# Kernel tuning notes

Measured on AMD Instinct MI355X. Metric: run time of the kernel, lower is better.

## Reference

```python
import jax, jax.numpy as jnp
import numpy as np

NU0 = 1.0  # nu0 temperature floor


def setup_inputs() -> dict:
    key = jax.random.key(0)
    ks = jax.random.split(key, 12)
    N, E, P, L, IN, H = 20000, 320000, 50000, 20, 128, 64
    xavier = lambda k, s: jax.random.normal(k, s, jnp.float32) * np.sqrt(2.0 / (s[0] + s[1]))
    return {
        "x": jax.random.normal(ks[0], (N, IN), jnp.float32),
        "edge_index": jax.random.randint(ks[1], (2, E), 0, N),
        "pairs": jax.random.randint(ks[2], (P, 2), 0, N),
        "gumbel": jax.random.gumbel(ks[3], (L, P, 2), jnp.float32),
        "W_enc": xavier(ks[4], (IN, H)),
        "Omega": xavier(ks[5], (H, H)),
        "Ws_raw": xavier(ks[6], (H, H)),
        "W_fc1": xavier(ks[7], (2 * H, 2 * H)),
        "W_fc2": xavier(ks[8], (2 * H, 2)),
        "W_fv": xavier(ks[9], (2 * H, 1)),
        "W_p1": xavier(ks[10], (2 * H, H)),
        "W_p2": xavier(ks[11], (H, 1)),
    }


def reference(x, edge_index, pairs, gumbel, W_enc, Omega, Ws_raw, W_fc1, W_fc2, W_fv, W_p1, W_p2):
    N = x.shape[0]
    src, dst = pairs[:, 0], pairs[:, 1]
    # add self loops
    loops = jnp.arange(N)
    row = jnp.concatenate([edge_index[0], loops])
    col = jnp.concatenate([edge_index[1], loops])
    deg = jax.ops.segment_sum(jnp.ones(col.shape, x.dtype), col, num_segments=N)
    dinv = jnp.where(deg > 0, deg, 1.0) ** -0.5 * (deg > 0)
    norm = dinv[row] * dinv[col]  # [E+N]
    Omega_as = Omega - Omega.T            # antisymmetric part
    W_s = (Ws_raw + Ws_raw.T) * 0.5       # symmetric part

    H = jax.nn.relu(x @ W_enc)                         # [N, h]
    r = jnp.concatenate([H[src], H[dst]], axis=-1)     # [P, 2h]
    ts0 = jnp.zeros(pairs.shape[0], x.dtype)

    def step(carry, g):
        H, r, ts = carry
        anti = -jax.nn.relu(H @ Omega_as)
        msg = (H @ W_s)[row] * norm[:, None]           # gather + weight
        sym = jax.ops.segment_sum(msg, col, num_segments=N)  # scatter-add
        dH = jax.nn.relu(jnp.tanh(anti + sym))
        huv = jnp.concatenate([H[src], H[dst]], axis=-1)     # [P, 2h]
        logits = jax.nn.relu(huv @ W_fc1) @ W_fc2            # [P, 2]
        nu = jax.nn.softplus(huv @ W_fv) + NU0               # [P, 1]
        c = jax.nn.softmax((logits + g) / nu, axis=-1)       # soft gumbel-softmax
        tau = c[:, :1]
        dr = jnp.concatenate([dH[src], dH[dst]], axis=-1)
        r = r + tau * dr
        H = H + dH
        ts = ts + jax.lax.stop_gradient(tau[:, 0])
        return (H, r, ts), None

    (H, r, ts), _ = jax.lax.scan(step, (H, r, ts0), gumbel)
    scores = (jax.nn.relu(r @ W_p1) @ W_p2)[:, 0]
    return scores, ts
```

## Files before the change

kernel.cpp:

```cpp
#include <hip/hip_runtime.h>
#include <math.h>


typedef short bf16x8 __attribute__((ext_vector_type(8)));
typedef float f32x4 __attribute__((ext_vector_type(4)));
typedef unsigned short u16x8 __attribute__((ext_vector_type(8)));

__device__ __forceinline__ float bf2f(unsigned short u) {
  return __uint_as_float(((unsigned)u) << 16);
}
__device__ __forceinline__ unsigned short f2bf(float f) {
  unsigned u = __float_as_uint(f);
  unsigned r = (u + 0x7FFFu + ((u >> 16) & 1u)) >> 16;
  return (unsigned short)r;
}
__device__ __forceinline__ float softplusf(float x) {
  return x > 20.f ? x : log1pf(expf(x));
}


__global__ void count_kernel(const int* __restrict__ col, int E, int* __restrict__ cnt) {
  int e = blockIdx.x * blockDim.x + threadIdx.x;
  if (e < E) atomicAdd(&cnt[col[e]], 1);
}

__global__ __launch_bounds__(1024) void scan1_kernel(int* __restrict__ cnt,
                                                     int* __restrict__ colptr,
                                                     float* __restrict__ dinv,
                                                     int* __restrict__ bsum, int N) {
  __shared__ int sh[1024];
  int t = threadIdx.x, b = blockIdx.x;
  int i = b * 1024 + t;
  int v = (i < N) ? cnt[i] : 0;
  sh[t] = v;
  __syncthreads();
  for (int off = 1; off < 1024; off <<= 1) {
    int o = (t >= off) ? sh[t - off] : 0;
    __syncthreads();
    sh[t] += o;
    __syncthreads();
  }
  if (i < N) {
    colptr[i] = sh[t] - v;
    dinv[i] = rsqrtf((float)(v + 1));
    cnt[i] = 0;
  }
  if (t == 1023) bsum[b] = sh[1023];
}

__global__ void scan2_kernel(int* __restrict__ bsum, int B) {
  if (threadIdx.x == 0 && blockIdx.x == 0) {
    int run = 0;
    for (int b = 0; b < B; b++) {
      int x = bsum[b];
      bsum[b] = run;
      run += x;
    }
    bsum[B] = run;
  }
}

__global__ void scan3_kernel(int* __restrict__ colptr, const int* __restrict__ bsum, int N) {
  int i = blockIdx.x * blockDim.x + threadIdx.x;
  if (i < N) colptr[i] += bsum[i >> 10];
  if (i == N) colptr[N] = bsum[(N + 1023) >> 10];
}

__global__ void fill_kernel(const int* __restrict__ row, const int* __restrict__ col, int E,
                            const int* __restrict__ colptr, int* __restrict__ cur,
                            int* __restrict__ csr) {
  int e = blockIdx.x * blockDim.x + threadIdx.x;
  if (e < E) {
    int c = col[e];
    int pos = colptr[c] + atomicAdd(&cur[c], 1);
    csr[pos] = row[e];
  }
}


__global__ void prep_weights(const float* __restrict__ Om, const float* __restrict__ Wsr,
                             const float* __restrict__ Wfc1, const float* __restrict__ Wenc,
                             const float* __restrict__ Wp1, unsigned short* __restrict__ Wn2T,
                             unsigned short* __restrict__ Wn2Tlo,
                             unsigned short* __restrict__ Wfc1T,
                             unsigned short* __restrict__ WencT,
                             unsigned short* __restrict__ Wp1T) {
  int idx = blockIdx.x * blockDim.x + threadIdx.x;
  if (idx < 128 * 64) {
    int j = idx / 64, k = idx % 64;
    float v;
    if (j < 64) {
      v = Om[k * 64 + j] - Om[j * 64 + k];
    } else {
      int jj = j - 64;
      v = 0.5f * (Wsr[k * 64 + jj] + Wsr[jj * 64 + k]);
    }
    unsigned short hi = f2bf(v);
    Wn2T[idx] = hi;
    Wn2Tlo[idx] = f2bf(v - bf2f(hi));
  } else if (idx < 128 * 64 + 128 * 128) {
    int t = idx - 128 * 64;
    int j = t / 128, k = t % 128;
    Wfc1T[t] = f2bf(Wfc1[k * 128 + j]);
  } else if (idx < 128 * 64 + 128 * 128 + 64 * 128) {
    int t = idx - 128 * 64 - 128 * 128;
    int j = t / 128, k = t % 128;
    WencT[t] = f2bf(Wenc[k * 64 + j]);
  } else if (idx < 128 * 64 + 128 * 128 + 2 * 64 * 128) {
    int t = idx - 128 * 64 - 128 * 128 - 64 * 128;
    int j = t / 128, k = t % 128;
    Wp1T[t] = f2bf(Wp1[k * 64 + j]);
  }
}


__global__ __launch_bounds__(256) void enc_gemm(const float* __restrict__ X,
                                                const unsigned short* __restrict__ WT,
                                                float* __restrict__ H, float* __restrict__ H0,
                                                unsigned short* __restrict__ Hb_hi,
                                                unsigned short* __restrict__ Hb_lo, int N) {
  int gw = blockIdx.x * 4 + (threadIdx.x >> 6);
  int l = threadIdx.x & 63;
  int r0 = gw * 16;
  if (r0 >= N) return;
  int arow = min(r0 + (l & 15), N - 1);
  int ak = (l >> 4) * 8;
  bf16x8 a[4];
#pragma unroll
  for (int kk = 0; kk < 4; kk++) {
    const float* xp = X + (size_t)arow * 128 + kk * 32 + ak;
    float4 u = *(const float4*)xp;
    float4 v = *(const float4*)(xp + 4);
    bf16x8 t;
    t[0] = (short)f2bf(u.x); t[1] = (short)f2bf(u.y);
    t[2] = (short)f2bf(u.z); t[3] = (short)f2bf(u.w);
    t[4] = (short)f2bf(v.x); t[5] = (short)f2bf(v.y);
    t[6] = (short)f2bf(v.z); t[7] = (short)f2bf(v.w);
    a[kk] = t;
  }
  int rbase = r0 + (l >> 4) * 4;
#pragma unroll
  for (int c = 0; c < 4; c++) {
    const unsigned short* wp = WT + (size_t)(c * 16 + (l & 15)) * 128 + ak;
    f32x4 acc = {0.f, 0.f, 0.f, 0.f};
#pragma unroll
    for (int kk = 0; kk < 4; kk++)
      acc = __builtin_amdgcn_mfma_f32_16x16x32_bf16(a[kk], *(const bf16x8*)(wp + kk * 32), acc,
                                                    0, 0, 0);
    int gcol = c * 16 + (l & 15);
#pragma unroll
    for (int b = 0; b < 4; b++) {
      int gr = rbase + b;
      if (gr < N) {
        float v = fmaxf(acc[b], 0.f);
        H[(size_t)gr * 64 + gcol] = v;
        H0[(size_t)gr * 64 + gcol] = v;
        unsigned short hi = f2bf(v);
        Hb_hi[(size_t)gr * 64 + gcol] = hi;
        Hb_lo[(size_t)gr * 64 + gcol] = f2bf(v - bf2f(hi));
      }
    }
  }
}


__global__ __launch_bounds__(256) void node_gemm(
    const unsigned short* __restrict__ Hb_hi, const unsigned short* __restrict__ Hb_lo,
    const unsigned short* __restrict__ Wn2T, const unsigned short* __restrict__ Wn2Tlo,
    const unsigned short* __restrict__ Wfc1T, const float* __restrict__ H,
    const float* __restrict__ Wfv, const float* __restrict__ dinv, float* __restrict__ Abuf,
    float* __restrict__ Bsbuf, float* __restrict__ Tbuf, float* __restrict__ Dbuf,
    float* __restrict__ ftfb, int N) {
  int gw = blockIdx.x * 4 + (threadIdx.x >> 6);
  int l = threadIdx.x & 63;
  int r0 = gw * 16;
  if (r0 >= N) return;
  int arow = min(r0 + (l & 15), N - 1);
  int ak = (l >> 4) * 8;
  bf16x8 a0h = *(const bf16x8*)(Hb_hi + (size_t)arow * 64 + ak);
  bf16x8 a1h = *(const bf16x8*)(Hb_hi + (size_t)arow * 64 + 32 + ak);
  bf16x8 a0l = *(const bf16x8*)(Hb_lo + (size_t)arow * 64 + ak);
  bf16x8 a1l = *(const bf16x8*)(Hb_lo + (size_t)arow * 64 + 32 + ak);
  int rbase = r0 + (l >> 4) * 4;
  float dv[4];
#pragma unroll
  for (int b = 0; b < 4; b++) dv[b] = dinv[min(rbase + b, N - 1)];
#pragma unroll
  for (int c = 0; c < 8; c++) {
    size_t woff = (size_t)(c * 16 + (l & 15)) * 64 + ak;
    bf16x8 b0h = *(const bf16x8*)(Wn2T + woff);
    bf16x8 b1h = *(const bf16x8*)(Wn2T + woff + 32);
    bf16x8 b0l = *(const bf16x8*)(Wn2Tlo + woff);
    bf16x8 b1l = *(const bf16x8*)(Wn2Tlo + woff + 32);
    f32x4 acc = {0.f, 0.f, 0.f, 0.f};
    acc = __builtin_amdgcn_mfma_f32_16x16x32_bf16(a0h, b0h, acc, 0, 0, 0);
    acc = __builtin_amdgcn_mfma_f32_16x16x32_bf16(a1h, b1h, acc, 0, 0, 0);
    acc = __builtin_amdgcn_mfma_f32_16x16x32_bf16(a0l, b0h, acc, 0, 0, 0);
    acc = __builtin_amdgcn_mfma_f32_16x16x32_bf16(a1l, b1h, acc, 0, 0, 0);
    acc = __builtin_amdgcn_mfma_f32_16x16x32_bf16(a0h, b0l, acc, 0, 0, 0);
    acc = __builtin_amdgcn_mfma_f32_16x16x32_bf16(a1h, b1l, acc, 0, 0, 0);
    int gcol = c * 16 + (l & 15);
#pragma unroll
    for (int b = 0; b < 4; b++) {
      int gr = rbase + b;
      if (gr < N) {
        float v = acc[b];
        if (c >= 4) Bsbuf[(size_t)gr * 64 + (gcol - 64)] = v * dv[b];
        else Abuf[(size_t)gr * 64 + gcol] = v;
      }
    }
  }
#pragma unroll
  for (int c = 0; c < 16; c++) {
    int j = ((c & 7) * 16 + (l & 15));
    int koff = (c < 8) ? 0 : 64;
    const unsigned short* wp = Wfc1T + (size_t)j * 128 + koff + ak;
    bf16x8 b0 = *(const bf16x8*)(wp);
    bf16x8 b1 = *(const bf16x8*)(wp + 32);
    f32x4 acc = {0.f, 0.f, 0.f, 0.f};
    acc = __builtin_amdgcn_mfma_f32_16x16x32_bf16(a0h, b0, acc, 0, 0, 0);
    acc = __builtin_amdgcn_mfma_f32_16x16x32_bf16(a1h, b1, acc, 0, 0, 0);
    acc = __builtin_amdgcn_mfma_f32_16x16x32_bf16(a0l, b0, acc, 0, 0, 0);
    acc = __builtin_amdgcn_mfma_f32_16x16x32_bf16(a1l, b1, acc, 0, 0, 0);
    float* dstb = (c < 8) ? Tbuf : Dbuf;
#pragma unroll
    for (int b = 0; b < 4; b++) {
      int gr = rbase + b;
      if (gr < N) dstb[(size_t)gr * 128 + j] = acc[b];
    }
  }
  int d0 = (l >> 4) * 16;
  const float* hp = H + (size_t)arow * 64 + d0;
  float p0 = 0.f, p1 = 0.f;
#pragma unroll
  for (int i = 0; i < 16; i += 4) {
    float4 h = *(const float4*)(hp + i);
    p0 += h.x * Wfv[d0 + i] + h.y * Wfv[d0 + i + 1] + h.z * Wfv[d0 + i + 2] +
          h.w * Wfv[d0 + i + 3];
    p1 += h.x * Wfv[64 + d0 + i] + h.y * Wfv[64 + d0 + i + 1] + h.z * Wfv[64 + d0 + i + 2] +
          h.w * Wfv[64 + d0 + i + 3];
  }
  p0 += __shfl_xor(p0, 16, 64);
  p0 += __shfl_xor(p0, 32, 64);
  p1 += __shfl_xor(p1, 16, 64);
  p1 += __shfl_xor(p1, 32, 64);
  if (l < 16 && r0 + l < N) {
    ftfb[2 * (r0 + l)] = p0;
    ftfb[2 * (r0 + l) + 1] = p1;
  }
}


__global__ __launch_bounds__(256) void step_fused(
    const float* __restrict__ A_cur, const float* __restrict__ Bs_cur,
    const float* __restrict__ T_cur, const float* __restrict__ D_cur,
    float* __restrict__ A_nxt, float* __restrict__ Bs_nxt, float* __restrict__ T_nxt,
    float* __restrict__ D_nxt, const int* __restrict__ colptr, const int* __restrict__ csr,
    const float* __restrict__ dinv, float* __restrict__ H, unsigned short* __restrict__ dHall,
    const unsigned short* __restrict__ Wn2T, const unsigned short* __restrict__ Wn2Tlo,
    const unsigned short* __restrict__ Wfc1T, const float* __restrict__ Wfc2,
    const float* __restrict__ ftfb_cur, float* __restrict__ ftfb_nxt,
    const float* __restrict__ Wfv, const int* __restrict__ pairs,
    const float* __restrict__ gum, float* __restrict__ tau, int t, int LT, int N, int P,
    int PB) {
  __shared__ unsigned short ldsHi[16 * 72];
  __shared__ unsigned short ldsLo[16 * 72];
  int l = threadIdx.x & 63;
  int w = threadIdx.x >> 6;
  if ((int)blockIdx.x < PB) {
    int p = (int)blockIdx.x * 32 + w * 8 + (l >> 3);
    bool act = p < P;
    int pc = act ? p : P - 1;
    int src = pairs[2 * pc], dst = pairs[2 * pc + 1];
    int d0 = (l & 7) * 16;
    const float* Tp = T_cur + (size_t)src * 128 + d0;
    const float* Dp = D_cur + (size_t)dst * 128 + d0;
    float l0 = 0.f, l1 = 0.f;
#pragma unroll
    for (int i = 0; i < 16; i += 4) {
      float4 tv = *(const float4*)(Tp + i);
      float4 dv4 = *(const float4*)(Dp + i);
      float z0 = fmaxf(tv.x + dv4.x, 0.f);
      float z1 = fmaxf(tv.y + dv4.y, 0.f);
      float z2 = fmaxf(tv.z + dv4.z, 0.f);
      float z3 = fmaxf(tv.w + dv4.w, 0.f);
      int m = d0 + i;
      l0 = fmaf(z0, Wfc2[2 * m], l0);
      l1 = fmaf(z0, Wfc2[2 * m + 1], l1);
      l0 = fmaf(z1, Wfc2[2 * m + 2], l0);
      l1 = fmaf(z1, Wfc2[2 * m + 3], l1);
      l0 = fmaf(z2, Wfc2[2 * m + 4], l0);
      l1 = fmaf(z2, Wfc2[2 * m + 5], l1);
      l0 = fmaf(z3, Wfc2[2 * m + 6], l0);
      l1 = fmaf(z3, Wfc2[2 * m + 7], l1);
    }
#pragma unroll
    for (int off = 1; off < 8; off <<= 1) {
      l0 += __shfl_xor(l0, off, 64);
      l1 += __shfl_xor(l1, off, 64);
    }
    if ((l & 7) == 0 && act) {
      float nu = softplusf(ftfb_cur[2 * src] + ftfb_cur[2 * dst + 1]) + 1.0f;
      float g0 = gum[2 * (size_t)p], g1 = gum[2 * (size_t)p + 1];
      float dlt = ((l1 + g1) - (l0 + g0)) / nu;
      tau[(size_t)p * LT + t] = 1.0f / (1.0f + expf(dlt));
    }
  } else {
    int nb0 = ((int)blockIdx.x - PB) * 16;
    int g = l >> 4;
    int node = nb0 + w * 4 + g;
    int q = (l & 15) * 4;
    bool valid = node < N;
    float4 hn = make_float4(0.f, 0.f, 0.f, 0.f);
    if (valid) {
      size_t base = (size_t)node * 64 + q;
      float4 v = *(const float4*)(Bs_cur + base);
      float aa0 = v.x, aa1 = v.y, aa2 = v.z, aa3 = v.w;
      int beg = colptr[node], end = colptr[node + 1];
      int i = beg;
      for (; i + 3 < end; i += 4) {
        int n0 = csr[i], n1 = csr[i + 1], n2 = csr[i + 2], n3 = csr[i + 3];
        float4 u0 = *(const float4*)(Bs_cur + (size_t)n0 * 64 + q);
        float4 u1 = *(const float4*)(Bs_cur + (size_t)n1 * 64 + q);
        float4 u2 = *(const float4*)(Bs_cur + (size_t)n2 * 64 + q);
        float4 u3 = *(const float4*)(Bs_cur + (size_t)n3 * 64 + q);
        aa0 += (u0.x + u1.x) + (u2.x + u3.x);
        aa1 += (u0.y + u1.y) + (u2.y + u3.y);
        aa2 += (u0.z + u1.z) + (u2.z + u3.z);
        aa3 += (u0.w + u1.w) + (u2.w + u3.w);
      }
      for (; i < end; i++) {
        int n0 = csr[i];
        float4 u0 = *(const float4*)(Bs_cur + (size_t)n0 * 64 + q);
        aa0 += u0.x; aa1 += u0.y; aa2 += u0.z; aa3 += u0.w;
      }
      float dval = dinv[node];
      float4 av = *(const float4*)(A_cur + base);
      float dh0 = fmaxf(tanhf(dval * aa0 - fmaxf(av.x, 0.f)), 0.f);
      float dh1 = fmaxf(tanhf(dval * aa1 - fmaxf(av.y, 0.f)), 0.f);
      float dh2 = fmaxf(tanhf(dval * aa2 - fmaxf(av.z, 0.f)), 0.f);
      float dh3 = fmaxf(tanhf(dval * aa3 - fmaxf(av.w, 0.f)), 0.f);
      ushort4 od;
      od.x = f2bf(dh0); od.y = f2bf(dh1); od.z = f2bf(dh2); od.w = f2bf(dh3);
      *(ushort4*)(dHall + (size_t)node * (LT * 64) + t * 64 + q) = od;
      float* hp = H + base;
      float4 h = *(const float4*)hp;
      hn.x = h.x + dh0; hn.y = h.y + dh1; hn.z = h.z + dh2; hn.w = h.w + dh3;
      *(float4*)hp = hn;
    }
    ushort4 whi, wlo;
    whi.x = f2bf(hn.x); wlo.x = f2bf(hn.x - bf2f(whi.x));
    whi.y = f2bf(hn.y); wlo.y = f2bf(hn.y - bf2f(whi.y));
    whi.z = f2bf(hn.z); wlo.z = f2bf(hn.z - bf2f(whi.z));
    whi.w = f2bf(hn.w); wlo.w = f2bf(hn.w - bf2f(whi.w));
    int r = w * 4 + g;
    *(ushort4*)(ldsHi + r * 72 + q) = whi;
    *(ushort4*)(ldsLo + r * 72 + q) = wlo;
    float p0 = hn.x * Wfv[q] + hn.y * Wfv[q + 1] + hn.z * Wfv[q + 2] + hn.w * Wfv[q + 3];
    float p1 = hn.x * Wfv[64 + q] + hn.y * Wfv[64 + q + 1] + hn.z * Wfv[64 + q + 2] +
               hn.w * Wfv[64 + q + 3];
#pragma unroll
    for (int off = 1; off < 16; off <<= 1) {
      p0 += __shfl_xor(p0, off, 64);
      p1 += __shfl_xor(p1, off, 64);
    }
    if ((l & 15) == 0 && valid) {
      ftfb_nxt[2 * node] = p0;
      ftfb_nxt[2 * node + 1] = p1;
    }
    __syncthreads();
    int rowA = l & 15;
    int ak = g * 8;
    bf16x8 a0h = *(const bf16x8*)(ldsHi + rowA * 72 + ak);
    bf16x8 a1h = *(const bf16x8*)(ldsHi + rowA * 72 + 32 + ak);
    bf16x8 a0l = *(const bf16x8*)(ldsLo + rowA * 72 + ak);
    bf16x8 a1l = *(const bf16x8*)(ldsLo + rowA * 72 + 32 + ak);
    float dv[4];
#pragma unroll
    for (int b = 0; b < 4; b++) dv[b] = dinv[min(nb0 + g * 4 + b, N - 1)];
#pragma unroll
    for (int cc = 0; cc < 2; cc++) {
      int c = cc * 4 + w;
      size_t woff = (size_t)(c * 16 + rowA) * 64 + ak;
      bf16x8 b0h = *(const bf16x8*)(Wn2T + woff);
      bf16x8 b1h = *(const bf16x8*)(Wn2T + woff + 32);
      bf16x8 b0l = *(const bf16x8*)(Wn2Tlo + woff);
      bf16x8 b1l = *(const bf16x8*)(Wn2Tlo + woff + 32);
      f32x4 acc = {0.f, 0.f, 0.f, 0.f};
      acc = __builtin_amdgcn_mfma_f32_16x16x32_bf16(a0h, b0h, acc, 0, 0, 0);
      acc = __builtin_amdgcn_mfma_f32_16x16x32_bf16(a1h, b1h, acc, 0, 0, 0);
      acc = __builtin_amdgcn_mfma_f32_16x16x32_bf16(a0l, b0h, acc, 0, 0, 0);
      acc = __builtin_amdgcn_mfma_f32_16x16x32_bf16(a1l, b1h, acc, 0, 0, 0);
      acc = __builtin_amdgcn_mfma_f32_16x16x32_bf16(a0h, b0l, acc, 0, 0, 0);
      acc = __builtin_amdgcn_mfma_f32_16x16x32_bf16(a1h, b1l, acc, 0, 0, 0);
      int gcol = c * 16 + rowA;
#pragma unroll
      for (int b = 0; b < 4; b++) {
        int gr = nb0 + g * 4 + b;
        if (gr < N) {
          float v = acc[b];
          if (cc == 1) Bs_nxt[(size_t)gr * 64 + (gcol - 64)] = v * dv[b];
          else A_nxt[(size_t)gr * 64 + gcol] = v;
        }
      }
    }
#pragma unroll
    for (int cc = 0; cc < 4; cc++) {
      int jb = (cc & 1) + 2 * w;
      int koff = (cc < 2) ? 0 : 64;
      int j = jb * 16 + rowA;
      const unsigned short* wp = Wfc1T + (size_t)j * 128 + koff + ak;
      bf16x8 b0 = *(const bf16x8*)(wp);
      bf16x8 b1 = *(const bf16x8*)(wp + 32);
      f32x4 acc = {0.f, 0.f, 0.f, 0.f};
      acc = __builtin_amdgcn_mfma_f32_16x16x32_bf16(a0h, b0, acc, 0, 0, 0);
      acc = __builtin_amdgcn_mfma_f32_16x16x32_bf16(a1h, b1, acc, 0, 0, 0);
      acc = __builtin_amdgcn_mfma_f32_16x16x32_bf16(a0l, b0, acc, 0, 0, 0);
      acc = __builtin_amdgcn_mfma_f32_16x16x32_bf16(a1l, b1, acc, 0, 0, 0);
      float* dstb = (cc < 2) ? T_nxt : D_nxt;
#pragma unroll
      for (int b = 0; b < 4; b++) {
        int gr = nb0 + g * 4 + b;
        if (gr < N) dstb[(size_t)gr * 128 + j] = acc[b];
      }
    }
  }
}


__global__ __launch_bounds__(256) void rbuild_kernel(
    const float* __restrict__ H0, const unsigned short* __restrict__ dHall,
    const float* __restrict__ tau, const int* __restrict__ pairs,
    unsigned short* __restrict__ rb_hi, unsigned short* __restrict__ rb_lo,
    float* __restrict__ ts, int P, int N, int Lsteps) {
  int p = blockIdx.x * 16 + (threadIdx.x >> 4);
  int l = threadIdx.x & 15;
  if (p >= P) return;
  int node = (l < 8) ? pairs[2 * p] : pairs[2 * p + 1];
  int d0 = (l & 7) * 8;
  const float* hp = H0 + (size_t)node * 64 + d0;
  float4 h0 = *(const float4*)hp;
  float4 h1 = *(const float4*)(hp + 4);
  float acc[8] = {h0.x, h0.y, h0.z, h0.w, h1.x, h1.y, h1.z, h1.w};
  float tsum = 0.f;
  const unsigned short* dbase = dHall + (size_t)node * (Lsteps * 64) + d0;
  const float* taup = tau + (size_t)p * Lsteps;
#pragma unroll 4
  for (int t = 0; t < Lsteps; t++) {
    float tt = taup[t];
    tsum += tt;
    u16x8 v = *(const u16x8*)(dbase + t * 64);
#pragma unroll
    for (int i = 0; i < 8; i++) acc[i] = fmaf(tt, bf2f(v[i]), acc[i]);
  }
  u16x8 ohi, olo;
#pragma unroll
  for (int i = 0; i < 8; i++) {
    unsigned short hi = f2bf(acc[i]);
    ohi[i] = hi;
    olo[i] = f2bf(acc[i] - bf2f(hi));
  }
  *(u16x8*)(rb_hi + (size_t)p * 128 + l * 8) = ohi;
  *(u16x8*)(rb_lo + (size_t)p * 128 + l * 8) = olo;
  if (l == 0) ts[p] = tsum;
}


__global__ __launch_bounds__(256) void final_gemm(const unsigned short* __restrict__ rb_hi,
                                                  const unsigned short* __restrict__ rb_lo,
                                                  const unsigned short* __restrict__ WT,
                                                  const float* __restrict__ Wp2,
                                                  float* __restrict__ out, int P) {
  int gw = blockIdx.x * 4 + (threadIdx.x >> 6);
  int l = threadIdx.x & 63;
  int r0 = gw * 16;
  if (r0 >= P) return;
  int arow = min(r0 + (l & 15), P - 1);
  int ak = (l >> 4) * 8;
  bf16x8 ah[4], al[4];
#pragma unroll
  for (int kk = 0; kk < 4; kk++) {
    ah[kk] = *(const bf16x8*)(rb_hi + (size_t)arow * 128 + kk * 32 + ak);
    al[kk] = *(const bf16x8*)(rb_lo + (size_t)arow * 128 + kk * 32 + ak);
  }
  float s[4] = {0.f, 0.f, 0.f, 0.f};
#pragma unroll
  for (int c = 0; c < 4; c++) {
    const unsigned short* wp = WT + (size_t)(c * 16 + (l & 15)) * 128 + ak;
    f32x4 acc = {0.f, 0.f, 0.f, 0.f};
#pragma unroll
    for (int kk = 0; kk < 4; kk++) {
      bf16x8 wv = *(const bf16x8*)(wp + kk * 32);
      acc = __builtin_amdgcn_mfma_f32_16x16x32_bf16(ah[kk], wv, acc, 0, 0, 0);
      acc = __builtin_amdgcn_mfma_f32_16x16x32_bf16(al[kk], wv, acc, 0, 0, 0);
    }
    float w = Wp2[c * 16 + (l & 15)];
#pragma unroll
    for (int b = 0; b < 4; b++) s[b] = fmaf(fmaxf(acc[b], 0.f), w, s[b]);
  }
#pragma unroll
  for (int off = 1; off < 16; off <<= 1) {
#pragma unroll
    for (int b = 0; b < 4; b++) s[b] += __shfl_xor(s[b], off, 64);
  }
  if ((l & 15) == 0) {
    int rbase = r0 + (l >> 4) * 4;
#pragma unroll
    for (int b = 0; b < 4; b++) {
      int gr = rbase + b;
      if (gr < P) out[gr] = s[b];
    }
  }
}


extern "C" void kernel_launch(void* const* d_in, const int* in_sizes, int n_in, void* d_out,
                              int out_size, void* d_ws, size_t ws_size, hipStream_t stream) {
  const float* x = (const float*)d_in[0];
  const int* edge = (const int*)d_in[1];
  const int* pairs = (const int*)d_in[2];
  const float* gumbel = (const float*)d_in[3];
  const float* Wenc = (const float*)d_in[4];
  const float* Om = (const float*)d_in[5];
  const float* Wsr = (const float*)d_in[6];
  const float* Wfc1 = (const float*)d_in[7];
  const float* Wfc2 = (const float*)d_in[8];
  const float* Wfv = (const float*)d_in[9];
  const float* Wp1 = (const float*)d_in[10];
  const float* Wp2 = (const float*)d_in[11];
  const int IN = 128;
  const int N = in_sizes[0] / IN;
  const int E = in_sizes[1] / 2;
  const int P = in_sizes[2] / 2;
  const int L = in_sizes[3] / (2 * P);
  float* out = (float*)d_out;

  char* wsb = (char*)d_ws;
  size_t off = 0;
  auto alloc = [&](size_t bytes) -> char* {
    char* p = wsb + off;
    off = (off + bytes + 255) & ~(size_t)255;
    return p;
  };
  const int NB = (N + 1023) >> 10;
  float* dinv = (float*)alloc((size_t)N * 4);
  int* cnt = (int*)alloc((size_t)N * 4);
  int* colptr = (int*)alloc((size_t)(N + 1) * 4);
  int* bsum = (int*)alloc((size_t)(NB + 1) * 4);
  int* csr = (int*)alloc((size_t)E * 4);
  unsigned short* Wn2T = (unsigned short*)alloc((size_t)128 * 64 * 2);
  unsigned short* Wn2Tlo = (unsigned short*)alloc((size_t)128 * 64 * 2);
  unsigned short* Wfc1T = (unsigned short*)alloc((size_t)128 * 128 * 2);
  unsigned short* WencT = (unsigned short*)alloc((size_t)64 * 128 * 2);
  unsigned short* Wp1T = (unsigned short*)alloc((size_t)64 * 128 * 2);
  float* H = (float*)alloc((size_t)N * 64 * 4);
  float* H0 = (float*)alloc((size_t)N * 64 * 4);
  unsigned short* Hb_hi = (unsigned short*)alloc((size_t)N * 64 * 2);
  unsigned short* Hb_lo = (unsigned short*)alloc((size_t)N * 64 * 2);
  float* A_a = (float*)alloc((size_t)N * 64 * 4);
  float* A_b = (float*)alloc((size_t)N * 64 * 4);
  float* Bs_a = (float*)alloc((size_t)N * 64 * 4);
  float* Bs_b = (float*)alloc((size_t)N * 64 * 4);
  float* T_a = (float*)alloc((size_t)N * 128 * 4);
  float* T_b = (float*)alloc((size_t)N * 128 * 4);
  float* D_a = (float*)alloc((size_t)N * 128 * 4);
  float* D_b = (float*)alloc((size_t)N * 128 * 4);
  float* ftfbA = (float*)alloc((size_t)N * 2 * 4);
  float* ftfbB = (float*)alloc((size_t)N * 2 * 4);
  unsigned short* dHall = (unsigned short*)alloc((size_t)N * L * 64 * 2);
  float* tau = (float*)alloc((size_t)P * L * 4);
  unsigned short* rb_hi = (unsigned short*)alloc((size_t)P * 128 * 2);
  unsigned short* rb_lo = (unsigned short*)alloc((size_t)P * 128 * 2);
  (void)ws_size;
  (void)n_in;
  (void)out_size;

  const int* erow = edge;
  const int* ecol = edge + E;

  hipMemsetAsync(cnt, 0, (size_t)N * 4, stream);
  count_kernel<<<(E + 255) / 256, 256, 0, stream>>>(ecol, E, cnt);
  scan1_kernel<<<NB, 1024, 0, stream>>>(cnt, colptr, dinv, bsum, N);
  scan2_kernel<<<1, 64, 0, stream>>>(bsum, NB);
  scan3_kernel<<<(N + 256) / 256, 256, 0, stream>>>(colptr, bsum, N);
  fill_kernel<<<(E + 255) / 256, 256, 0, stream>>>(erow, ecol, E, colptr, cnt, csr);
  prep_weights<<<(128 * 64 + 128 * 128 + 2 * 64 * 128 + 255) / 256, 256, 0, stream>>>(
      Om, Wsr, Wfc1, Wenc, Wp1, Wn2T, Wn2Tlo, Wfc1T, WencT, Wp1T);

  int nwaves = (N + 15) / 16;
  enc_gemm<<<(nwaves + 3) / 4, 256, 0, stream>>>(x, WencT, H, H0, Hb_hi, Hb_lo, N);
  node_gemm<<<(nwaves + 3) / 4, 256, 0, stream>>>(Hb_hi, Hb_lo, Wn2T, Wn2Tlo, Wfc1T, H, Wfv,
                                                  dinv, A_a, Bs_a, T_a, D_a, ftfbA, N);

  float* A_cur = A_a;   float* A_nxt = A_b;
  float* Bs_cur = Bs_a; float* Bs_nxt = Bs_b;
  float* T_cur = T_a;   float* T_nxt = T_b;
  float* D_cur = D_a;   float* D_nxt = D_b;
  float* ff_cur = ftfbA;
  float* ff_nxt = ftfbB;
  const int PB = (P + 31) / 32;
  const int AGB = (N + 15) / 16;
  for (int t = 0; t < L; t++) {
    step_fused<<<PB + AGB, 256, 0, stream>>>(
        A_cur, Bs_cur, T_cur, D_cur, A_nxt, Bs_nxt, T_nxt, D_nxt, colptr, csr, dinv, H, dHall,
        Wn2T, Wn2Tlo, Wfc1T, Wfc2, ff_cur, ff_nxt, Wfv, pairs, gumbel + (size_t)t * P * 2, tau,
        t, L, N, P, PB);
    { float* tmp = A_cur; A_cur = A_nxt; A_nxt = tmp; }
    { float* tmp = Bs_cur; Bs_cur = Bs_nxt; Bs_nxt = tmp; }
    { float* tmp = T_cur; T_cur = T_nxt; T_nxt = tmp; }
    { float* tmp = D_cur; D_cur = D_nxt; D_nxt = tmp; }
    { float* tmp = ff_cur; ff_cur = ff_nxt; ff_nxt = tmp; }
  }
  rbuild_kernel<<<(P + 15) / 16, 256, 0, stream>>>(H0, dHall, tau, pairs, rb_hi, rb_lo,
                                                   out + P, P, N, L);
  int pwaves = (P + 15) / 16;
  final_gemm<<<(pwaves + 3) / 4, 256, 0, stream>>>(rb_hi, rb_lo, Wp1T, Wp2, out, P);
}
```

Measured before the change: 917.4 us.

## Sort pairs by source node and fuse r-build with final projection GEMM

Builds a counting-sort permutation of pairs by source node (extra count/scan/fill kernels) and has the per-step pair blocks and the final kernel walk pairs in that order. This makes gathers of T/D/dHall rows for the same source more cache-local. It also fuses rbuild and final_gemm so r stays in LDS instead of a global hi/lo round trip. The cost is extra setup launches and an indirection load per pair, plus scattered writes to outputs and tau.

Result: no change. 908.7 us (-0.9%).

```diff
diff --git a/kernel.cpp b/kernel.cpp
--- a/kernel.cpp
+++ b/kernel.cpp
@@ -22,6 +22,11 @@
 __global__ void count_kernel(const int* __restrict__ col, int E, int* __restrict__ cnt) {
   int e = blockIdx.x * blockDim.x + threadIdx.x;
   if (e < E) atomicAdd(&cnt[col[e]], 1);
+}
+
+__global__ void pcount_kernel(const int* __restrict__ pairs, int P, int* __restrict__ cnt) {
+  int p = blockIdx.x * blockDim.x + threadIdx.x;
+  if (p < P) atomicAdd(&cnt[pairs[2 * p]], 1);
 }
 
 __global__ __launch_bounds__(1024) void scan1_kernel(int* __restrict__ cnt,
@@ -42,7 +47,7 @@
   }
   if (i < N) {
     colptr[i] = sh[t] - v;
-    dinv[i] = rsqrtf((float)(v + 1));
+    if (dinv) dinv[i] = rsqrtf((float)(v + 1));
     cnt[i] = 0;
   }
   if (t == 1023) bsum[b] = sh[1023];
@@ -74,6 +79,17 @@
     int c = col[e];
     int pos = colptr[c] + atomicAdd(&cur[c], 1);
     csr[pos] = row[e];
+  }
+}
+
+__global__ void pfill_kernel(const int* __restrict__ pairs, int P,
+                             const int* __restrict__ pptr, int* __restrict__ pcur,
+                             int* __restrict__ porder) {
+  int p = blockIdx.x * blockDim.x + threadIdx.x;
+  if (p < P) {
+    int s = pairs[2 * p];
+    int pos = pptr[s] + atomicAdd(&pcur[s], 1);
+    porder[pos] = p;
   }
 }
 
@@ -261,17 +277,17 @@
     const unsigned short* __restrict__ Wfc1T, const float* __restrict__ Wfc2,
     const float* __restrict__ ftfb_cur, float* __restrict__ ftfb_nxt,
     const float* __restrict__ Wfv, const int* __restrict__ pairs,
-    const float* __restrict__ gum, float* __restrict__ tau, int t, int LT, int N, int P,
-    int PB) {
+    const int* __restrict__ porder, const float* __restrict__ gum, float* __restrict__ tau,
+    int t, int LT, int N, int P, int PB) {
   __shared__ unsigned short ldsHi[16 * 72];
   __shared__ unsigned short ldsLo[16 * 72];
   int l = threadIdx.x & 63;
   int w = threadIdx.x >> 6;
   if ((int)blockIdx.x < PB) {
-    int p = (int)blockIdx.x * 32 + w * 8 + (l >> 3);
-    bool act = p < P;
-    int pc = act ? p : P - 1;
-    int src = pairs[2 * pc], dst = pairs[2 * pc + 1];
+    int idx = (int)blockIdx.x * 32 + w * 8 + (l >> 3);
+    bool act = idx < P;
+    int p = porder[act ? idx : P - 1];
+    int src = pairs[2 * p], dst = pairs[2 * p + 1];
     int d0 = (l & 7) * 16;
     const float* Tp = T_cur + (size_t)src * 128 + d0;
     const float* Dp = D_cur + (size_t)dst * 128 + d0;
@@ -428,16 +444,28 @@
 }
 
 
-__global__ __launch_bounds__(256) void rbuild_kernel(
+__global__ __launch_bounds__(256) void rbuild_final(
     const float* __restrict__ H0, const unsigned short* __restrict__ dHall,
     const float* __restrict__ tau, const int* __restrict__ pairs,
-    unsigned short* __restrict__ rb_hi, unsigned short* __restrict__ rb_lo,
-    float* __restrict__ ts, int P, int N, int Lsteps) {
-  int p = blockIdx.x * 16 + (threadIdx.x >> 4);
-  int l = threadIdx.x & 15;
-  if (p >= P) return;
-  int node = (l < 8) ? pairs[2 * p] : pairs[2 * p + 1];
-  int d0 = (l & 7) * 8;
+    const int* __restrict__ porder, const unsigned short* __restrict__ Wp1T,
+    const float* __restrict__ Wp2, float* __restrict__ out, float* __restrict__ ts, int P,
+    int N, int Lsteps) {
+  __shared__ unsigned short sHi[16 * 136];
+  __shared__ unsigned short sLo[16 * 136];
+  __shared__ float sS[4][16];
+  __shared__ int sP[16];
+  __shared__ int sV[16];
+  int pr = threadIdx.x >> 4;
+  int l16 = threadIdx.x & 15;
+  int i0 = (int)blockIdx.x * 16;
+  bool act = (i0 + pr) < P;
+  int p = porder[act ? (i0 + pr) : P - 1];
+  if (l16 == 0) {
+    sP[pr] = p;
+    sV[pr] = act ? 1 : 0;
+  }
+  int node = (l16 < 8) ? pairs[2 * p] : pairs[2 * p + 1];
+  int d0 = (l16 & 7) * 8;
   const float* hp = H0 + (size_t)node * 64 + d0;
   float4 h0 = *(const float4*)hp;
   float4 h1 = *(const float4*)(hp + 4);
@@ -460,56 +488,46 @@
     ohi[i] = hi;
     olo[i] = f2bf(acc[i] - bf2f(hi));
   }
-  *(u16x8*)(rb_hi + (size_t)p * 128 + l * 8) = ohi;
-  *(u16x8*)(rb_lo + (size_t)p * 128 + l * 8) = olo;
-  if (l == 0) ts[p] = tsum;
-}
-
-
-__global__ __launch_bounds__(256) void final_gemm(const unsigned short* __restrict__ rb_hi,
-                                                  const unsigned short* __restrict__ rb_lo,
-                                                  const unsigned short* __restrict__ WT,
-                                                  const float* __restrict__ Wp2,
-                                                  float* __restrict__ out, int P) {
-  int gw = blockIdx.x * 4 + (threadIdx.x >> 6);
+  *(u16x8*)(sHi + pr * 136 + l16 * 8) = ohi;
+  *(u16x8*)(sLo + pr * 136 + l16 * 8) = olo;
+  if (l16 == 0 && act) ts[p] = tsum;
+  __syncthreads();
+  int w = threadIdx.x >> 6;
   int l = threadIdx.x & 63;
-  int r0 = gw * 16;
-  if (r0 >= P) return;
-  int arow = min(r0 + (l & 15), P - 1);
+  int rowA = l & 15;
   int ak = (l >> 4) * 8;
   bf16x8 ah[4], al[4];
 #pragma unroll
   for (int kk = 0; kk < 4; kk++) {
-    ah[kk] = *(const bf16x8*)(rb_hi + (size_t)arow * 128 + kk * 32 + ak);
-    al[kk] = *(const bf16x8*)(rb_lo + (size_t)arow * 128 + kk * 32 + ak);
-  }
-  float s[4] = {0.f, 0.f, 0.f, 0.f};
-#pragma unroll
-  for (int c = 0; c < 4; c++) {
-    const unsigned short* wp = WT + (size_t)(c * 16 + (l & 15)) * 128 + ak;
-    f32x4 acc = {0.f, 0.f, 0.f, 0.f};
-#pragma unroll
-    for (int kk = 0; kk < 4; kk++) {
-      bf16x8 wv = *(const bf16x8*)(wp + kk * 32);
-      acc = __builtin_amdgcn_mfma_f32_16x16x32_bf16(ah[kk], wv, acc, 0, 0, 0);
-      acc = __builtin_amdgcn_mfma_f32_16x16x32_bf16(al[kk], wv, acc, 0, 0, 0);
-    }
-    float w = Wp2[c * 16 + (l & 15)];
-#pragma unroll
-    for (int b = 0; b < 4; b++) s[b] = fmaf(fmaxf(acc[b], 0.f), w, s[b]);
-  }
+    ah[kk] = *(const bf16x8*)(sHi + rowA * 136 + kk * 32 + ak);
+    al[kk] = *(const bf16x8*)(sLo + rowA * 136 + kk * 32 + ak);
+  }
+  const unsigned short* wp = Wp1T + (size_t)(w * 16 + rowA) * 128 + ak;
+  f32x4 macc = {0.f, 0.f, 0.f, 0.f};
+#pragma unroll
+  for (int kk = 0; kk < 4; kk++) {
+    bf16x8 wv = *(const bf16x8*)(wp + kk * 32);
+    macc = __builtin_amdgcn_mfma_f32_16x16x32_bf16(ah[kk], wv, macc, 0, 0, 0);
+    macc = __builtin_amdgcn_mfma_f32_16x16x32_bf16(al[kk], wv, macc, 0, 0, 0);
+  }
+  float wcol = Wp2[w * 16 + rowA];
+  float s[4];
+#pragma unroll
+  for (int b = 0; b < 4; b++) s[b] = fmaxf(macc[b], 0.f) * wcol;
 #pragma unroll
   for (int off = 1; off < 16; off <<= 1) {
 #pragma unroll
     for (int b = 0; b < 4; b++) s[b] += __shfl_xor(s[b], off, 64);
   }
   if ((l & 15) == 0) {
-    int rbase = r0 + (l >> 4) * 4;
-#pragma unroll
-    for (int b = 0; b < 4; b++) {
-      int gr = rbase + b;
-      if (gr < P) out[gr] = s[b];
-    }
+#pragma unroll
+    for (int b = 0; b < 4; b++) sS[w][(l >> 4) * 4 + b] = s[b];
+  }
+  __syncthreads();
+  if (threadIdx.x < 16) {
+    int row = threadIdx.x;
+    float sum = sS[0][row] + sS[1][row] + sS[2][row] + sS[3][row];
+    if (sV[row]) out[sP[row]] = sum;
   }
 }
 
@@ -548,6 +566,10 @@
   int* colptr = (int*)alloc((size_t)(N + 1) * 4);
   int* bsum = (int*)alloc((size_t)(NB + 1) * 4);
   int* csr = (int*)alloc((size_t)E * 4);
+  int* pcnt = (int*)alloc((size_t)N * 4);
+  int* pptr = (int*)alloc((size_t)(N + 1) * 4);
+  int* pbsum = (int*)alloc((size_t)(NB + 1) * 4);
+  int* porder = (int*)alloc((size_t)P * 4);
   unsigned short* Wn2T = (unsigned short*)alloc((size_t)128 * 64 * 2);
   unsigned short* Wn2Tlo = (unsigned short*)alloc((size_t)128 * 64 * 2);
   unsigned short* Wfc1T = (unsigned short*)alloc((size_t)128 * 128 * 2);
@@ -569,8 +591,6 @@
   float* ftfbB = (float*)alloc((size_t)N * 2 * 4);
   unsigned short* dHall = (unsigned short*)alloc((size_t)N * L * 64 * 2);
   float* tau = (float*)alloc((size_t)P * L * 4);
-  unsigned short* rb_hi = (unsigned short*)alloc((size_t)P * 128 * 2);
-  unsigned short* rb_lo = (unsigned short*)alloc((size_t)P * 128 * 2);
   (void)ws_size;
   (void)n_in;
   (void)out_size;
@@ -579,11 +599,17 @@
   const int* ecol = edge + E;
 
   hipMemsetAsync(cnt, 0, (size_t)N * 4, stream);
+  hipMemsetAsync(pcnt, 0, (size_t)N * 4, stream);
   count_kernel<<<(E + 255) / 256, 256, 0, stream>>>(ecol, E, cnt);
+  pcount_kernel<<<(P + 255) / 256, 256, 0, stream>>>(pairs, P, pcnt);
   scan1_kernel<<<NB, 1024, 0, stream>>>(cnt, colptr, dinv, bsum, N);
+  scan1_kernel<<<NB, 1024, 0, stream>>>(pcnt, pptr, nullptr, pbsum, N);
   scan2_kernel<<<1, 64, 0, stream>>>(bsum, NB);
+  scan2_kernel<<<1, 64, 0, stream>>>(pbsum, NB);
   scan3_kernel<<<(N + 256) / 256, 256, 0, stream>>>(colptr, bsum, N);
+  scan3_kernel<<<(N + 256) / 256, 256, 0, stream>>>(pptr, pbsum, N);
   fill_kernel<<<(E + 255) / 256, 256, 0, stream>>>(erow, ecol, E, colptr, cnt, csr);
+  pfill_kernel<<<(P + 255) / 256, 256, 0, stream>>>(pairs, P, pptr, pcnt, porder);
   prep_weights<<<(128 * 64 + 128 * 128 + 2 * 64 * 128 + 255) / 256, 256, 0, stream>>>(
       Om, Wsr, Wfc1, Wenc, Wp1, Wn2T, Wn2Tlo, Wfc1T, WencT, Wp1T);
 
@@ -603,16 +629,14 @@
   for (int t = 0; t < L; t++) {
     step_fused<<<PB + AGB, 256, 0, stream>>>(
         A_cur, Bs_cur, T_cur, D_cur, A_nxt, Bs_nxt, T_nxt, D_nxt, colptr, csr, dinv, H, dHall,
-        Wn2T, Wn2Tlo, Wfc1T, Wfc2, ff_cur, ff_nxt, Wfv, pairs, gumbel + (size_t)t * P * 2, tau,
-        t, L, N, P, PB);
+        Wn2T, Wn2Tlo, Wfc1T, Wfc2, ff_cur, ff_nxt, Wfv, pairs, porder,
+        gumbel + (size_t)t * P * 2, tau, t, L, N, P, PB);
     { float* tmp = A_cur; A_cur = A_nxt; A_nxt = tmp; }
     { float* tmp = Bs_cur; Bs_cur = Bs_nxt; Bs_nxt = tmp; }
     { float* tmp = T_cur; T_cur = T_nxt; T_nxt = tmp; }
     { float* tmp = D_cur; D_cur = D_nxt; D_nxt = tmp; }
     { float* tmp = ff_cur; ff_cur = ff_nxt; ff_nxt = tmp; }
   }
-  rbuild_kernel<<<(P + 15) / 16, 256, 0, stream>>>(H0, dHall, tau, pairs, rb_hi, rb_lo,
-                                                   out + P, P, N, L);
-  int pwaves = (P + 15) / 16;
-  final_gemm<<<(pwaves + 3) / 4, 256, 0, stream>>>(rb_hi, rb_lo, Wp1T, Wp2, out, P);
-}
+  rbuild_final<<<(P + 15) / 16, 256, 0, stream>>>(H0, dHall, tau, pairs, porder, Wp1T, Wp2,
+                                                  out, out + P, P, N, L);
+}
```
